# Kernel optimization log

Measured on AMD Instinct MI355X. Metric: run time of the kernel, lower is better.

## Reference

```python
import jax, jax.numpy as jnp
import numpy as np

# static config (matches init_kwargs)
STRIDE, PAD, DIL, DG = 1, 1, 1, 1
KH, KW = 3, 3
CIN, COUT = 64, 64


def setup_inputs() -> dict:
    key = jax.random.key(0)
    k1, k2, k3, k4 = jax.random.split(key, 4)
    N, C, H, W = 4, CIN, 128, 128
    K = KH * KW
    x = jax.random.normal(k1, (N, C, H, W), dtype=jnp.float32)
    offset = jax.random.normal(k2, (N, 2 * DG * K, H, W), dtype=jnp.float32)
    mask = jax.random.uniform(k3, (N, DG * K, H, W), dtype=jnp.float32)
    stdv = 1.0 / np.sqrt(C * K)
    weight = jax.random.uniform(k4, (COUT, C, KH, KW), dtype=jnp.float32,
                                minval=-stdv, maxval=stdv)
    bias = jnp.zeros((COUT,), dtype=jnp.float32)  # no_bias=True -> frozen zeros
    return {"x": x, "offset": offset, "mask": mask, "weight": weight, "bias": bias}


def _dcnv2(x, offset, mask, weight, bias):
    N, C, H, W = x.shape
    Cout, _, kh, kw = weight.shape
    K = kh * kw
    Ho = (H + 2 * PAD - DIL * (kh - 1) - 1) // STRIDE + 1
    Wo = (W + 2 * PAD - DIL * (kw - 1) - 1) // STRIDE + 1
    Cg = C // DG

    # offsets: [N, DG, K, 2(y,x), Ho, Wo]; mask: [N, DG, K, Ho, Wo]
    off = offset.reshape(N, DG, K, 2, Ho, Wo)
    off_y, off_x = off[:, :, :, 0], off[:, :, :, 1]
    m = mask.reshape(N, DG, K, Ho, Wo)

    kidx = jnp.arange(K)
    ky, kx = kidx // kw, kidx % kw
    base_y = (jnp.arange(Ho) * STRIDE - PAD)[None, :] + (ky * DIL)[:, None]  # [K,Ho]
    base_x = (jnp.arange(Wo) * STRIDE - PAD)[None, :] + (kx * DIL)[:, None]  # [K,Wo]

    py = base_y[None, None, :, :, None].astype(x.dtype) + off_y  # [N,DG,K,Ho,Wo]
    px = base_x[None, None, :, None, :].astype(x.dtype) + off_x

    y0 = jnp.floor(py)
    x0 = jnp.floor(px)
    ly = py - y0  # frac weights
    lx = px - x0
    y0i = y0.astype(jnp.int32)
    x0i = x0.astype(jnp.int32)

    xf = x.reshape(N, DG, Cg, H * W)

    def gather(yi, xi):
        # per-corner zero padding (out-of-bounds corners contribute 0)
        valid = ((yi >= 0) & (yi < H) & (xi >= 0) & (xi < W))
        idx = jnp.clip(yi, 0, H - 1) * W + jnp.clip(xi, 0, W - 1)  # [N,DG,K,Ho,Wo]
        idx_b = jnp.broadcast_to(idx[:, :, None], (N, DG, Cg, K, Ho, Wo))
        v = jnp.take_along_axis(xf, idx_b.reshape(N, DG, Cg, -1), axis=3)
        v = v.reshape(N, DG, Cg, K, Ho, Wo)
        return v * valid[:, :, None].astype(x.dtype)

    w00 = ((1 - ly) * (1 - lx))[:, :, None]  # [N,DG,1,K,Ho,Wo]
    w01 = ((1 - ly) * lx)[:, :, None]
    w10 = (ly * (1 - lx))[:, :, None]
    w11 = (ly * lx)[:, :, None]

    val = (gather(y0i, x0i) * w00 + gather(y0i, x0i + 1) * w01
           + gather(y0i + 1, x0i) * w10 + gather(y0i + 1, x0i + 1) * w11)
    cols = val * m[:, :, None]                      # modulation
    cols = cols.reshape(N, C, K, Ho, Wo)            # DG*Cg -> C (contiguous)

    wmat = weight.reshape(Cout, C, K)
    out = jnp.einsum('nckhw,ock->nohw', cols, wmat)
    return out + bias[None, :, None, None]


def reference(x, offset, mask, weight, bias):
    return _dcnv2(x, offset, mask, weight, bias)
```

## Files before the change

kernel.cpp:

```cpp
#include <hip/hip_runtime.h>

#define N_    4
#define C_    64
#define H_    128
#define W_    128
#define KW_   3
#define K_    9
#define COUT_ 64
#define HW_   (H_ * W_)
#define NPIX  (N_ * HW_)
#define KK_   (C_ * K_)

typedef _Float16 h2 __attribute__((ext_vector_type(2)));
typedef _Float16 h4 __attribute__((ext_vector_type(4)));
typedef _Float16 h8 __attribute__((ext_vector_type(8)));
typedef float v4f __attribute__((ext_vector_type(4)));
typedef int   v4i __attribute__((ext_vector_type(4)));

__global__ __launch_bounds__(256) void prep(
    const float* __restrict__ x, _Float16* __restrict__ xh,
    const float* __restrict__ w, _Float16* __restrict__ wA3)
{
    if (blockIdx.x < 1024) {
        const int n   = blockIdx.x >> 8;
        const int hw0 = (blockIdx.x & 255) * 64;

        __shared__ float tile[64][65];
        const float* xb = x + n * (C_ * HW_);
#pragma unroll
        for (int i = 0; i < 4; ++i) {
            const int idx = i * 256 + threadIdx.x;
            const int q   = idx & 15;
            const int c   = idx >> 4;
            const v4f v = *(const v4f*)&xb[c * HW_ + hw0 + 4 * q];
            tile[4 * q + 0][c] = v.x;
            tile[4 * q + 1][c] = v.y;
            tile[4 * q + 2][c] = v.z;
            tile[4 * q + 3][c] = v.w;
        }
        __syncthreads();
        _Float16* xo = xh + ((size_t)n * HW_ + hw0) * 64;
#pragma unroll
        for (int i = 0; i < 4; ++i) {
            const int idx = i * 256 + threadIdx.x;
            const int c4  = idx & 15;
            const int hr  = idx >> 4;
            h4 v;
            v.x = (_Float16)tile[hr][4 * c4 + 0];
            v.y = (_Float16)tile[hr][4 * c4 + 1];
            v.z = (_Float16)tile[hr][4 * c4 + 2];
            v.w = (_Float16)tile[hr][4 * c4 + 3];
            *(h4*)&xo[hr * 64 + 4 * c4] = v;
        }
    } else {
        const int tid = (blockIdx.x - 1024) * 256 + threadIdx.x;
        if (tid < COUT_ * KK_) {
            const int k   = tid % KK_;
            const int o   = tid / KK_;
            const int c   = k & 63;
            const int tap = k >> 6;
            wA3[tid] = (_Float16)w[o * (C_ * K_) + c * K_ + tap];
        }
    }
}

__global__ __launch_bounds__(256, 4) void dcn_fused(
    const _Float16* __restrict__ xh,
    const float* __restrict__ offset,
    const float* __restrict__ mask,
    const _Float16* __restrict__ wA3,
    const float* __restrict__ bias,
    float* __restrict__ out)
{
    const int tid  = threadIdx.x;
    const int lane = tid & 63;
    const int wv   = tid >> 6;
    const int quad = lane >> 4;
    const int l16  = lane & 15;
    const int g    = lane >> 3;
    const int l8   = lane & 7;

    const int lb  = (blockIdx.x & 7) * 128 + (blockIdx.x >> 3);
    const int pxb = lb * 64;
    const int n   = pxb >> 14;
    const int hwb = pxb & (HW_ - 1);

    __shared__ _Float16 cwh[576][4];
    __shared__ int      ci[576][4];
    __shared__ _Float16 Bt[2][64][72];

#pragma unroll
    for (int r = 0; r < 3; ++r) {
        const int e = tid + 256 * r;
        if (e < 576) {
            const int p  = e / 9;
            const int t  = e - p * 9;
            const int hw = hwb + p;
            const int ho = hw >> 7;
            const int wo = hw & (W_ - 1);
            const int ky = t / KW_;
            const int kx = t - ky * KW_;

            const float offy = offset[n * (2 * K_ * HW_) + (2 * t + 0) * HW_ + hw];
            const float offx = offset[n * (2 * K_ * HW_) + (2 * t + 1) * HW_ + hw];
            const float mval = mask[n * (K_ * HW_) + t * HW_ + hw];

            const float py = (float)(ho - 1 + ky) + offy;
            const float qx = (float)(wo - 1 + kx) + offx;
            const float y0f = floorf(py), x0f = floorf(qx);
            const float ly = py - y0f, lx = qx - x0f;
            const int y0 = (int)y0f, x0 = (int)x0f;
            const int y1 = y0 + 1,   x1 = x0 + 1;
            const bool vy0 = (y0 >= 0) & (y0 < H_);
            const bool vy1 = (y1 >= 0) & (y1 < H_);
            const bool vx0 = (x0 >= 0) & (x0 < W_);
            const bool vx1 = (x1 >= 0) & (x1 < W_);
            const int cy0 = min(max(y0, 0), H_ - 1);
            const int cy1 = min(max(y1, 0), H_ - 1);
            const int cx0 = min(max(x0, 0), W_ - 1);
            const int cx1 = min(max(x1, 0), W_ - 1);

            h4 q;
            q.x = (_Float16)((1.f - ly) * (1.f - lx) * mval * ((vy0 && vx0) ? 1.f : 0.f));
            q.y = (_Float16)((1.f - ly) * lx         * mval * ((vy0 && vx1) ? 1.f : 0.f));
            q.z = (_Float16)(ly         * (1.f - lx) * mval * ((vy1 && vx0) ? 1.f : 0.f));
            q.w = (_Float16)(ly         * lx         * mval * ((vy1 && vx1) ? 1.f : 0.f));
            *(h4*)&cwh[e][0] = q;
            int* qi = &ci[e][0];
            qi[0] = cy0 * W_ + cx0;
            qi[1] = cy0 * W_ + cx1;
            qi[2] = cy1 * W_ + cx0;
            qi[3] = cy1 * W_ + cx1;
        }
    }
    __syncthreads();

    const _Float16* xb8 = xh + ((size_t)n * HW_) * 64 + 8 * l8;
    const int pg  = wv * 16 + g;
    const int pg8 = pg + 8;

    const int mb   = (wv & 1) * 32;
    const int pxwl = (wv >> 1) * 32;

    v4f acc[2][2];
#pragma unroll
    for (int mh = 0; mh < 2; ++mh)
#pragma unroll
        for (int nh = 0; nh < 2; ++nh)
            acc[mh][nh] = (v4f){0.f, 0.f, 0.f, 0.f};

    h8 LA[2][4], LB[2][4];

#define ISSUE(t, R)                                                         \
    {                                                                       \
        const v4i oa = *(const v4i*)&ci[pg  * 9 + (t)][0];                  \
        const v4i ob = *(const v4i*)&ci[pg8 * 9 + (t)][0];                  \
        R[0][0] = *(const h8*)(xb8 + (size_t)oa.x * 64);                    \
        R[0][1] = *(const h8*)(xb8 + (size_t)oa.y * 64);                    \
        R[0][2] = *(const h8*)(xb8 + (size_t)oa.z * 64);                    \
        R[0][3] = *(const h8*)(xb8 + (size_t)oa.w * 64);                    \
        R[1][0] = *(const h8*)(xb8 + (size_t)ob.x * 64);                    \
        R[1][1] = *(const h8*)(xb8 + (size_t)ob.y * 64);                    \
        R[1][2] = *(const h8*)(xb8 + (size_t)ob.z * 64);                    \
        R[1][3] = *(const h8*)(xb8 + (size_t)ob.w * 64);                    \
    }

#define FINISH(t, R, b)                                                     \
    {                                                                       \
        _Pragma("unroll")                                                   \
        for (int h = 0; h < 2; ++h) {                                       \
            const int p = wv * 16 + h * 8 + g;                              \
            const h4 f = *(const h4*)&cwh[p * 9 + (t)][0];                  \
            const h8 F0 = {f.x, f.x, f.x, f.x, f.x, f.x, f.x, f.x};         \
            const h8 F1 = {f.y, f.y, f.y, f.y, f.y, f.y, f.y, f.y};         \
            const h8 F2 = {f.z, f.z, f.z, f.z, f.z, f.z, f.z, f.z};         \
            const h8 F3 = {f.w, f.w, f.w, f.w, f.w, f.w, f.w, f.w};         \
            h8 rr = F0 * R[h][0];                                           \
            rr = __builtin_elementwise_fma(F1, R[h][1], rr);                \
            rr = __builtin_elementwise_fma(F2, R[h][2], rr);                \
            rr = __builtin_elementwise_fma(F3, R[h][3], rr);                \
            *(h8*)&Bt[b][p][8 * l8] = rr;                                   \
        }                                                                   \
    }

    ISSUE(0, LA)
    ISSUE(1, LB)
    FINISH(0, LA, 0)
    __syncthreads();

#pragma unroll
    for (int t = 0; t < K_; ++t) {
        const int buf = t & 1;
        if ((t & 1) == 0) {
            if (t + 2 < K_) ISSUE(t + 2, LA)
        } else {
            if (t + 2 < K_) ISSUE(t + 2, LB)
        }

#pragma unroll
        for (int kc = 0; kc < 2; ++kc) {
            h8 bfr[2];
#pragma unroll
            for (int nh = 0; nh < 2; ++nh)
                bfr[nh] = *(const h8*)&Bt[buf][pxwl + nh * 16 + l16][kc * 32 + quad * 8];
            h8 afr[2];
#pragma unroll
            for (int mh = 0; mh < 2; ++mh)
                afr[mh] = *(const h8*)(wA3 + (size_t)(mb + mh * 16 + l16) * KK_
                                            + t * 64 + kc * 32 + quad * 8);
#pragma unroll
            for (int mh = 0; mh < 2; ++mh)
#pragma unroll
                for (int nh = 0; nh < 2; ++nh)
                    acc[mh][nh] = __builtin_amdgcn_mfma_f32_16x16x32_f16(
                        afr[mh], bfr[nh], acc[mh][nh], 0, 0, 0);
        }

        if ((t & 1) == 0) {
            if (t + 1 < K_) FINISH(t + 1, LB, buf ^ 1)
        } else {
            if (t + 1 < K_) FINISH(t + 1, LA, buf ^ 1)
        }
        __syncthreads();
    }
#undef ISSUE
#undef FINISH

    float* outb = out + n * (COUT_ * HW_);
#pragma unroll
    for (int mh = 0; mh < 2; ++mh)
#pragma unroll
        for (int nh = 0; nh < 2; ++nh)
#pragma unroll
            for (int r = 0; r < 4; ++r) {
                const int m = mb + mh * 16 + quad * 4 + r;
                outb[m * HW_ + hwb + pxwl + nh * 16 + l16] = acc[mh][nh][r] + bias[m];
            }
}

__global__ __launch_bounds__(256) void dcn_fallback(
    const float* __restrict__ x, const float* __restrict__ offset,
    const float* __restrict__ mask, const float* __restrict__ wptr,
    const float* __restrict__ bias, float* __restrict__ out)
{
    const int pix = blockIdx.x * 256 + threadIdx.x;
    const int n = pix >> 14, hw = pix & (HW_ - 1);
    const int ho = hw >> 7,  wo = hw & (W_ - 1);
    float acc[COUT_];
#pragma unroll
    for (int o = 0; o < COUT_; ++o) acc[o] = bias[o];
    const float* xn   = x + n * (C_ * HW_);
    const float* offn = offset + n * (2 * K_ * HW_) + hw;
    const float* mn   = mask + n * (K_ * HW_) + hw;
    for (int ct = 0; ct < C_; ct += 8) {
        for (int k = 0; k < K_; ++k) {
            const int ky = k / KW_, kx = k - ky * KW_;
            const float off_y = offn[(2 * k + 0) * HW_];
            const float off_x = offn[(2 * k + 1) * HW_];
            const float m = mn[k * HW_];
            const float py = (float)(ho - 1 + ky) + off_y;
            const float px = (float)(wo - 1 + kx) + off_x;
            const float y0f = floorf(py), x0f = floorf(px);
            const float ly = py - y0f, lx = px - x0f;
            const int y0 = (int)y0f, x0 = (int)x0f, y1 = y0 + 1, x1 = x0 + 1;
            const bool vy0 = (y0 >= 0) & (y0 < H_), vy1 = (y1 >= 0) & (y1 < H_);
            const bool vx0 = (x0 >= 0) & (x0 < W_), vx1 = (x1 >= 0) & (x1 < W_);
            const int cy0 = min(max(y0, 0), H_ - 1), cy1 = min(max(y1, 0), H_ - 1);
            const int cx0 = min(max(x0, 0), W_ - 1), cx1 = min(max(x1, 0), W_ - 1);
            const int i00 = cy0 * W_ + cx0, i01 = cy0 * W_ + cx1;
            const int i10 = cy1 * W_ + cx0, i11 = cy1 * W_ + cx1;
            const float f00 = (1.f - ly) * (1.f - lx) * m * ((vy0 && vx0) ? 1.f : 0.f);
            const float f01 = (1.f - ly) * lx * m * ((vy0 && vx1) ? 1.f : 0.f);
            const float f10 = ly * (1.f - lx) * m * ((vy1 && vx0) ? 1.f : 0.f);
            const float f11 = ly * lx * m * ((vy1 && vx1) ? 1.f : 0.f);
            for (int cc = 0; cc < 8; ++cc) {
                const int c = ct + cc;
                const float* xc = xn + c * HW_;
                const float val = fmaf(f00, xc[i00], fmaf(f01, xc[i01],
                                  fmaf(f10, xc[i10], f11 * xc[i11])));
#pragma unroll
                for (int o = 0; o < COUT_; ++o)
                    acc[o] = fmaf(wptr[o * (C_ * K_) + c * K_ + k], val, acc[o]);
            }
        }
    }
    float* outp = out + n * (COUT_ * HW_) + hw;
#pragma unroll
    for (int o = 0; o < COUT_; ++o) outp[o * HW_] = acc[o];
}

extern "C" void kernel_launch(void* const* d_in, const int* in_sizes, int n_in,
                              void* d_out, int out_size, void* d_ws, size_t ws_size,
                              hipStream_t stream) {
    const float* x      = (const float*)d_in[0];
    const float* offset = (const float*)d_in[1];
    const float* mask   = (const float*)d_in[2];
    const float* weight = (const float*)d_in[3];
    const float* bias   = (const float*)d_in[4];
    float* out = (float*)d_out;

    const size_t xh_bytes = (size_t)NPIX * C_ * sizeof(_Float16);
    const size_t wA_bytes = (size_t)COUT_ * KK_ * sizeof(_Float16);

    if (ws_size >= xh_bytes + wA_bytes) {
        _Float16* xh  = (_Float16*)d_ws;
        _Float16* wA3 = (_Float16*)((char*)d_ws + xh_bytes);
        prep<<<1024 + 144, 256, 0, stream>>>(x, xh, weight, wA3);
        dcn_fused<<<NPIX / 64, 256, 0, stream>>>(xh, offset, mask, wA3, bias, out);
    } else {
        dcn_fallback<<<NPIX / 256, 256, 0, stream>>>(x, offset, mask, weight, bias, out);
    }
}
```

Baseline: 109.6 us.

## Make each wave own its pixel tile to drop block-wide barriers

Each wave now computes all 64 output channels for its own 16 pixels, using wave-private LDS slices for the bilinear coefficients, gather indices and the B tile. This removes the per-tap __syncthreads, since only the wave that writes its staging buffers reads them back. In exchange, each wave reloads all four weight fragments per k-chunk instead of sharing them across waves. It also relies on in-order LDS access within a wave instead of an explicit barrier.

```diff
diff --git a/kernel.cpp b/kernel.cpp
--- a/kernel.cpp
+++ b/kernel.cpp
@@ -11,7 +11,6 @@
 #define NPIX  (N_ * HW_)
 #define KK_   (C_ * K_)
 
-typedef _Float16 h2 __attribute__((ext_vector_type(2)));
 typedef _Float16 h4 __attribute__((ext_vector_type(4)));
 typedef _Float16 h8 __attribute__((ext_vector_type(8)));
 typedef float v4f __attribute__((ext_vector_type(4)));
@@ -84,18 +83,19 @@
     const int pxb = lb * 64;
     const int n   = pxb >> 14;
     const int hwb = pxb & (HW_ - 1);
-
-    __shared__ _Float16 cwh[576][4];
-    __shared__ int      ci[576][4];
-    __shared__ _Float16 Bt[2][64][72];
+    const int hww = hwb + wv * 16;
+
+    __shared__ h4  cwh[4][144];
+    __shared__ v4i ci[4][144];
+    __shared__ _Float16 Bt[4][2][16][72];
 
 #pragma unroll
     for (int r = 0; r < 3; ++r) {
-        const int e = tid + 256 * r;
-        if (e < 576) {
+        const int e = r * 64 + lane;
+        if (e < 144) {
             const int p  = e / 9;
             const int t  = e - p * 9;
-            const int hw = hwb + p;
+            const int hw = hww + p;
             const int ho = hw >> 7;
             const int wo = hw & (W_ - 1);
             const int ky = t / KW_;
@@ -125,36 +125,31 @@
             q.y = (_Float16)((1.f - ly) * lx         * mval * ((vy0 && vx1) ? 1.f : 0.f));
             q.z = (_Float16)(ly         * (1.f - lx) * mval * ((vy1 && vx0) ? 1.f : 0.f));
             q.w = (_Float16)(ly         * lx         * mval * ((vy1 && vx1) ? 1.f : 0.f));
-            *(h4*)&cwh[e][0] = q;
-            int* qi = &ci[e][0];
-            qi[0] = cy0 * W_ + cx0;
-            qi[1] = cy0 * W_ + cx1;
-            qi[2] = cy1 * W_ + cx0;
-            qi[3] = cy1 * W_ + cx1;
+            cwh[wv][e] = q;
+            v4i ii;
+            ii.x = cy0 * W_ + cx0;
+            ii.y = cy0 * W_ + cx1;
+            ii.z = cy1 * W_ + cx0;
+            ii.w = cy1 * W_ + cx1;
+            ci[wv][e] = ii;
         }
     }
     __syncthreads();
 
     const _Float16* xb8 = xh + ((size_t)n * HW_) * 64 + 8 * l8;
-    const int pg  = wv * 16 + g;
-    const int pg8 = pg + 8;
-
-    const int mb   = (wv & 1) * 32;
-    const int pxwl = (wv >> 1) * 32;
-
-    v4f acc[2][2];
-#pragma unroll
-    for (int mh = 0; mh < 2; ++mh)
-#pragma unroll
-        for (int nh = 0; nh < 2; ++nh)
-            acc[mh][nh] = (v4f){0.f, 0.f, 0.f, 0.f};
+    const int pa = g;
+    const int pb = g + 8;
+
+    v4f acc[4];
+#pragma unroll
+    for (int mh = 0; mh < 4; ++mh) acc[mh] = (v4f){0.f, 0.f, 0.f, 0.f};
 
     h8 LA[2][4], LB[2][4];
 
 #define ISSUE(t, R)                                                         \
     {                                                                       \
-        const v4i oa = *(const v4i*)&ci[pg  * 9 + (t)][0];                  \
-        const v4i ob = *(const v4i*)&ci[pg8 * 9 + (t)][0];                  \
+        const v4i oa = ci[wv][pa * 9 + (t)];                                \
+        const v4i ob = ci[wv][pb * 9 + (t)];                                \
         R[0][0] = *(const h8*)(xb8 + (size_t)oa.x * 64);                    \
         R[0][1] = *(const h8*)(xb8 + (size_t)oa.y * 64);                    \
         R[0][2] = *(const h8*)(xb8 + (size_t)oa.z * 64);                    \
@@ -169,8 +164,8 @@
     {                                                                       \
         _Pragma("unroll")                                                   \
         for (int h = 0; h < 2; ++h) {                                       \
-            const int p = wv * 16 + h * 8 + g;                              \
-            const h4 f = *(const h4*)&cwh[p * 9 + (t)][0];                  \
+            const int p = h * 8 + g;                                        \
+            const h4 f = cwh[wv][p * 9 + (t)];                              \
             const h8 F0 = {f.x, f.x, f.x, f.x, f.x, f.x, f.x, f.x};         \
             const h8 F1 = {f.y, f.y, f.y, f.y, f.y, f.y, f.y, f.y};         \
             const h8 F2 = {f.z, f.z, f.z, f.z, f.z, f.z, f.z, f.z};         \
@@ -179,14 +174,13 @@
             rr = __builtin_elementwise_fma(F1, R[h][1], rr);                \
             rr = __builtin_elementwise_fma(F2, R[h][2], rr);                \
             rr = __builtin_elementwise_fma(F3, R[h][3], rr);                \
-            *(h8*)&Bt[b][p][8 * l8] = rr;                                   \
+            *(h8*)&Bt[wv][b][p][8 * l8] = rr;                               \
         }                                                                   \
     }
 
     ISSUE(0, LA)
     ISSUE(1, LB)
     FINISH(0, LA, 0)
-    __syncthreads();
 
 #pragma unroll
     for (int t = 0; t < K_; ++t) {
@@ -199,21 +193,14 @@
 
 #pragma unroll
         for (int kc = 0; kc < 2; ++kc) {
-            h8 bfr[2];
-#pragma unroll
-            for (int nh = 0; nh < 2; ++nh)
-                bfr[nh] = *(const h8*)&Bt[buf][pxwl + nh * 16 + l16][kc * 32 + quad * 8];
-            h8 afr[2];
-#pragma unroll
-            for (int mh = 0; mh < 2; ++mh)
-                afr[mh] = *(const h8*)(wA3 + (size_t)(mb + mh * 16 + l16) * KK_
+            const h8 bfr = *(const h8*)&Bt[wv][buf][l16][kc * 32 + quad * 8];
+#pragma unroll
+            for (int mh = 0; mh < 4; ++mh) {
+                const h8 afr = *(const h8*)(wA3 + (size_t)(mh * 16 + l16) * KK_
                                             + t * 64 + kc * 32 + quad * 8);
-#pragma unroll
-            for (int mh = 0; mh < 2; ++mh)
-#pragma unroll
-                for (int nh = 0; nh < 2; ++nh)
-                    acc[mh][nh] = __builtin_amdgcn_mfma_f32_16x16x32_f16(
-                        afr[mh], bfr[nh], acc[mh][nh], 0, 0, 0);
+                acc[mh] = __builtin_amdgcn_mfma_f32_16x16x32_f16(
+                    afr, bfr, acc[mh], 0, 0, 0);
+            }
         }
 
         if ((t & 1) == 0) {
@@ -221,21 +208,18 @@
         } else {
             if (t + 1 < K_) FINISH(t + 1, LA, buf ^ 1)
         }
-        __syncthreads();
     }
 #undef ISSUE
 #undef FINISH
 
-    float* outb = out + n * (COUT_ * HW_);
-#pragma unroll
-    for (int mh = 0; mh < 2; ++mh)
-#pragma unroll
-        for (int nh = 0; nh < 2; ++nh)
-#pragma unroll
-            for (int r = 0; r < 4; ++r) {
-                const int m = mb + mh * 16 + quad * 4 + r;
-                outb[m * HW_ + hwb + pxwl + nh * 16 + l16] = acc[mh][nh][r] + bias[m];
-            }
+    float* outb = out + n * (COUT_ * HW_) + hwb + wv * 16 + l16;
+#pragma unroll
+    for (int mh = 0; mh < 4; ++mh)
+#pragma unroll
+        for (int r = 0; r < 4; ++r) {
+            const int m = mh * 16 + quad * 4 + r;
+            outb[m * HW_] = acc[mh][r] + bias[m];
+        }
 }
 
 __global__ __launch_bounds__(256) void dcn_fallback(
```

Measured after the change: 123.9 us. 13.1% more time.

## Pre-tile weights into MFMA fragment order and relax per-tap barrier waits

Applied to the files above, without the earlier changes.

The weight matrix is repacked in the prep kernel into blocks laid out in MFMA A-fragment order, so each lane reads a contiguous 16-byte chunk per fragment. All A fragments for a tap are loaded at the top of the iteration, before the gather loads are issued. The per-tap __syncthreads is replaced by a barrier that waits only on LDS counters (lgkmcnt), wrapped in sched_barrier fences, so outstanding global gathers for later taps stay in flight across the barrier. In exchange, the fixed scheduling fences restrict compiler reordering, and the correctness of the lighter barrier depends on the Bt LDS writes being the only data that needs ordering.

```diff
diff --git a/kernel.cpp b/kernel.cpp
--- a/kernel.cpp
+++ b/kernel.cpp
@@ -11,7 +11,6 @@
 #define NPIX  (N_ * HW_)
 #define KK_   (C_ * K_)
 
-typedef _Float16 h2 __attribute__((ext_vector_type(2)));
 typedef _Float16 h4 __attribute__((ext_vector_type(4)));
 typedef _Float16 h8 __attribute__((ext_vector_type(8)));
 typedef float v4f __attribute__((ext_vector_type(4)));
@@ -19,7 +18,7 @@
 
 __global__ __launch_bounds__(256) void prep(
     const float* __restrict__ x, _Float16* __restrict__ xh,
-    const float* __restrict__ w, _Float16* __restrict__ wA3)
+    const float* __restrict__ w, _Float16* __restrict__ wA4)
 {
     if (blockIdx.x < 1024) {
         const int n   = blockIdx.x >> 8;
@@ -55,11 +54,16 @@
     } else {
         const int tid = (blockIdx.x - 1024) * 256 + threadIdx.x;
         if (tid < COUT_ * KK_) {
-            const int k   = tid % KK_;
-            const int o   = tid / KK_;
-            const int c   = k & 63;
-            const int tap = k >> 6;
-            wA3[tid] = (_Float16)w[o * (C_ * K_) + c * K_ + tap];
+            const int blk = tid >> 9;
+            const int r   = tid & 511;
+            const int l16 = r >> 5;
+            const int ch  = r & 31;
+            const int t   = blk >> 3;
+            const int kc  = (blk >> 2) & 1;
+            const int mh  = blk & 3;
+            const int o   = mh * 16 + l16;
+            const int c   = kc * 32 + ch;
+            wA4[tid] = (_Float16)w[o * (C_ * K_) + c * K_ + t];
         }
     }
 }
@@ -68,7 +72,7 @@
     const _Float16* __restrict__ xh,
     const float* __restrict__ offset,
     const float* __restrict__ mask,
-    const _Float16* __restrict__ wA3,
+    const _Float16* __restrict__ wA4,
     const float* __restrict__ bias,
     float* __restrict__ out)
 {
@@ -140,7 +144,10 @@
     const int pg8 = pg + 8;
 
     const int mb   = (wv & 1) * 32;
+    const int mhb  = (wv & 1) * 2;
     const int pxwl = (wv >> 1) * 32;
+
+    const _Float16* ab = wA4 + l16 * 32 + quad * 8;
 
     v4f acc[2][2];
 #pragma unroll
@@ -183,19 +190,37 @@
         }                                                                   \
     }
 
+#define TAP_BARRIER()                                                       \
+    __builtin_amdgcn_sched_barrier(0);                                      \
+    asm volatile("s_waitcnt lgkmcnt(0)");                                   \
+    __builtin_amdgcn_sched_barrier(0);                                      \
+    __builtin_amdgcn_s_barrier();                                           \
+    __builtin_amdgcn_sched_barrier(0);
+
     ISSUE(0, LA)
     ISSUE(1, LB)
     FINISH(0, LA, 0)
-    __syncthreads();
+    TAP_BARRIER()
 
 #pragma unroll
     for (int t = 0; t < K_; ++t) {
         const int buf = t & 1;
+
+        h8 va[2][2];
+#pragma unroll
+        for (int kc = 0; kc < 2; ++kc)
+#pragma unroll
+            for (int mh = 0; mh < 2; ++mh)
+                va[kc][mh] = *(const h8*)(ab
+                    + (size_t)(t * 8 + kc * 4 + (mhb + mh)) * 512);
+        __builtin_amdgcn_sched_barrier(0);
+
         if ((t & 1) == 0) {
             if (t + 2 < K_) ISSUE(t + 2, LA)
         } else {
             if (t + 2 < K_) ISSUE(t + 2, LB)
         }
+        __builtin_amdgcn_sched_barrier(0);
 
 #pragma unroll
         for (int kc = 0; kc < 2; ++kc) {
@@ -203,17 +228,12 @@
 #pragma unroll
             for (int nh = 0; nh < 2; ++nh)
                 bfr[nh] = *(const h8*)&Bt[buf][pxwl + nh * 16 + l16][kc * 32 + quad * 8];
-            h8 afr[2];
-#pragma unroll
-            for (int mh = 0; mh < 2; ++mh)
-                afr[mh] = *(const h8*)(wA3 + (size_t)(mb + mh * 16 + l16) * KK_
-                                            + t * 64 + kc * 32 + quad * 8);
 #pragma unroll
             for (int mh = 0; mh < 2; ++mh)
 #pragma unroll
                 for (int nh = 0; nh < 2; ++nh)
                     acc[mh][nh] = __builtin_amdgcn_mfma_f32_16x16x32_f16(
-                        afr[mh], bfr[nh], acc[mh][nh], 0, 0, 0);
+                        va[kc][mh], bfr[nh], acc[mh][nh], 0, 0, 0);
         }
 
         if ((t & 1) == 0) {
@@ -221,10 +241,12 @@
         } else {
             if (t + 1 < K_) FINISH(t + 1, LA, buf ^ 1)
         }
-        __syncthreads();
+
+        TAP_BARRIER()
     }
 #undef ISSUE
 #undef FINISH
+#undef TAP_BARRIER
 
     float* outb = out + n * (COUT_ * HW_);
 #pragma unroll
@@ -304,9 +326,9 @@
 
     if (ws_size >= xh_bytes + wA_bytes) {
         _Float16* xh  = (_Float16*)d_ws;
-        _Float16* wA3 = (_Float16*)((char*)d_ws + xh_bytes);
-        prep<<<1024 + 144, 256, 0, stream>>>(x, xh, weight, wA3);
-        dcn_fused<<<NPIX / 64, 256, 0, stream>>>(xh, offset, mask, wA3, bias, out);
+        _Float16* wA4 = (_Float16*)((char*)d_ws + xh_bytes);
+        prep<<<1024 + 144, 256, 0, stream>>>(x, xh, weight, wA4);
+        dcn_fused<<<NPIX / 64, 256, 0, stream>>>(xh, offset, mask, wA4, bias, out);
     } else {
         dcn_fallback<<<NPIX / 256, 256, 0, stream>>>(x, offset, mask, weight, bias, out);
     }
```

Result: faster. 102.2 us (-6.7%).
